# Optimization experiments

Hardware: AMD Instinct MI355X
Metric: run time of the kernel (lower is better)

The kernel has to match this reference:

```python
import jax, jax.numpy as jnp
import numpy as np

B, S, D = 16, 2048, 256

def setup_inputs() -> dict:
    key = jax.random.key(0)
    ks = jax.random.split(key, 7)
    scale = 1.0 / np.sqrt(D)
    return {
        "x": jax.random.normal(ks[0], (B, S, D), dtype=jnp.float32),
        "Wq": jax.random.normal(ks[1], (D, D), dtype=jnp.float32) * scale,
        "bq": jax.random.normal(ks[2], (D,), dtype=jnp.float32) * 0.01,
        "Wk": jax.random.normal(ks[3], (D, D), dtype=jnp.float32) * scale,
        "bk": jax.random.normal(ks[4], (D,), dtype=jnp.float32) * 0.01,
        "Wv": jax.random.normal(ks[5], (D, D), dtype=jnp.float32) * scale,
        "bv": jax.random.normal(ks[6], (D,), dtype=jnp.float32) * 0.01,
    }

def reference(x, Wq, bq, Wk, bk, Wv, bv):
    # q,k,v: [B,S,D]
    q = x @ Wq + bq
    k = x @ Wk + bk
    v = x @ Wv + bv
    inv_sqrt_d = jnp.asarray(1.0 / np.sqrt(x.shape[-1]), dtype=x.dtype)
    energy = jnp.einsum('bqd,bkd->bqk', q, k) * inv_sqrt_d  # [B,S,S]
    attn = jax.nn.softmax(energy, axis=-1)
    weighted = jnp.einsum('bqk,bkd->bqd', attn, v)  # [B,S,D]
    return weighted.sum(axis=1)  # [B,D]
```

## Files before the change

### kernel.cpp

```cpp
#include <hip/hip_runtime.h>
#include <hip/hip_bf16.h>

typedef __bf16 bf16_t;
typedef bf16_t bf16x8 __attribute__((ext_vector_type(8)));
typedef bf16_t bf16x4 __attribute__((ext_vector_type(4)));
typedef float  f32x4  __attribute__((ext_vector_type(4)));

constexpr int S = 2048, D = 256;


__device__ __forceinline__ float fast_exp2(float x) {
    return __builtin_amdgcn_exp2f(x);
}

__global__ void wt_kernel(const float* __restrict__ Wq, const float* __restrict__ Wk,
                          bf16_t* __restrict__ wtf) {
    int idx = blockIdx.x * 256 + threadIdx.x;
    int w    = idx >> 13;
    int rem  = idx & 8191;
    int nt   = rem >> 9;
    int rem2 = rem & 511;
    int ks   = rem2 >> 6;
    int lane = rem2 & 63;
    int lm = lane & 15, lg = lane >> 4;
    const float* Wsrc = (w == 0) ? Wq : Wk;
    int col = nt * 16 + lm, krow = ks * 32 + lg * 8;
    bf16x8 o;
#pragma unroll
    for (int j = 0; j < 8; j++) o[j] = (bf16_t)Wsrc[(krow + j) * 256 + col];
    *(bf16x8*)(wtf + (size_t)idx * 8) = o;
}

__global__ __launch_bounds__(256) void xconv_kernel(
    const float* __restrict__ x, bf16_t* __restrict__ xf) {
    __shared__ bf16_t xt[4][4096];
    int tid = threadIdx.x, wave = tid >> 6, lane = tid & 63;
    int qb = blockIdx.x * 4 + wave;
    const float* xr = x + (size_t)qb * 16 * 256;
    bf16_t* buf = xt[wave];
    int ks = lane >> 3, lg = (lane & 7) >> 1, j = (lane & 1) * 4;
#pragma unroll
    for (int rr = 0; rr < 16; rr++) {
        float4 f = *(const float4*)(xr + rr * 256 + lane * 4);
        bf16x4 o;
        o[0] = (bf16_t)f.x; o[1] = (bf16_t)f.y; o[2] = (bf16_t)f.z; o[3] = (bf16_t)f.w;
        *(bf16x4*)&buf[(ks * 64 + lg * 16 + rr) * 8 + j] = o;
    }
    bf16_t* dst = xf + (size_t)qb * 4096;
#pragma unroll
    for (int k2 = 0; k2 < 8; k2++) {
        bf16x8 v = *(const bf16x8*)&buf[k2 * 512 + lane * 8];
        *(bf16x8*)(dst + k2 * 512 + lane * 8) = v;
    }
}

__global__ __launch_bounds__(256, 2) void proj_kernel(
    const bf16_t* __restrict__ xf, const bf16_t* __restrict__ wtf,
    const float* __restrict__ bq, const float* __restrict__ bk,
    bf16_t* __restrict__ qo, bf16_t* __restrict__ ko) {
    __shared__ bf16_t bst[32768];
    __shared__ bf16_t sb_all[4][1152];
    int w    = blockIdx.y;
    int tid  = threadIdx.x;
    int wave = tid >> 6, lane = tid & 63, lm = lane & 15, lg = lane >> 4;
    int rowb = blockIdx.x >> 1;
    int colh = blockIdx.x & 1;
    int rowg = wave >> 1, colg = wave & 1;
    const float* bias = (w == 0) ? bq : bk;

    {
        const bf16_t* src = wtf + w * 65536 + (size_t)colh * 32768;
#pragma unroll
        for (int rnd = 0; rnd < 4; rnd++) {
            bf16x8 tmp[4];
#pragma unroll
            for (int u = 0; u < 4; u++)
                tmp[u] = *(const bf16x8*)(src + (size_t)((rnd * 4 + u) * 256 + tid) * 8);
#pragma unroll
            for (int u = 0; u < 4; u++)
                *(bf16x8*)&bst[(size_t)((rnd * 4 + u) * 256 + tid) * 8] = tmp[u];
        }
    }

    int qb0 = rowb * 8 + rowg * 4;
    bf16x8 af[4][8];
#pragma unroll
    for (int s = 0; s < 4; s++) {
        const bf16_t* ab = xf + (size_t)(qb0 + s) * 4096;
#pragma unroll
        for (int ks = 0; ks < 8; ks++)
            af[s][ks] = *(const bf16x8*)(ab + ks * 512 + lane * 8);
    }
    __syncthreads();

    f32x4 acc[4][4];
#pragma unroll
    for (int s = 0; s < 4; s++)
#pragma unroll
        for (int nt = 0; nt < 4; nt++) acc[s][nt] = f32x4{0.f, 0.f, 0.f, 0.f};
#pragma unroll
    for (int ks = 0; ks < 8; ks++) {
#pragma unroll
        for (int nt = 0; nt < 4; nt++) {
            bf16x8 bfr = *(const bf16x8*)&bst[(size_t)(((colg * 4 + nt) * 8 + ks) * 512) + lane * 8];
#pragma unroll
            for (int s = 0; s < 4; s++)
                acc[s][nt] = __builtin_amdgcn_mfma_f32_16x16x32_bf16(af[s][ks], bfr, acc[s][nt], 0, 0, 0);
        }
    }

    bf16_t* sb = sb_all[wave];
    bf16_t* dst = (w == 0) ? qo : ko;
    int c0 = colh * 128 + colg * 64;
#pragma unroll
    for (int s = 0; s < 4; s++) {
#pragma unroll
        for (int nt = 0; nt < 4; nt++) {
            int colloc = nt * 16 + lm;
            float bval = bias[c0 + colloc];
#pragma unroll
            for (int r = 0; r < 4; r++)
                sb[(lg * 4 + r) * 72 + colloc] = (bf16_t)(acc[s][nt][r] + bval);
        }
#pragma unroll
        for (int kk = 0; kk < 2; kk++) {
            bf16x8 v8 = *(const bf16x8*)&sb[lm * 72 + kk * 32 + lg * 8];
            *(bf16x8*)(dst + ((size_t)((qb0 + s) * 8 + (c0 >> 5) + kk)) * 512 + lane * 8) = v8;
        }
    }
}

template <int PASS>
__global__ __launch_bounds__(512, 2) void attn_pass(
    const bf16_t* __restrict__ q, const bf16_t* __restrict__ kmat,
    float* __restrict__ lpart, float* __restrict__ wpart) {
    __shared__ bf16_t wacc[8][512];

    int tid  = threadIdx.x;
    int wave = tid >> 6, lane = tid & 63, lm = lane & 15, lg = lane >> 4;
    int i    = blockIdx.x;
    int idx2 = i >> 3;
    int qt   = idx2 & 3;
    int kh   = (idx2 >> 2) & 3;
    int b    = (i & 7) * 2 + (idx2 >> 4);

    bf16x8 af[4][8];
#pragma unroll
    for (int s = 0; s < 4; s++) {
        const bf16_t* qb = q + ((size_t)((b * 128 + qt * 32 + wave * 4 + s) * 8)) * 512;
#pragma unroll
        for (int ks = 0; ks < 8; ks++)
            af[s][ks] = *(const bf16x8*)(qb + ks * 512 + lane * 8);
    }

    constexpr float SCL = 0.0625f * 1.44269504f;

    float lr[4][4];
    if (PASS == 2) {
#pragma unroll
        for (int s = 0; s < 4; s++)
#pragma unroll
            for (int r = 0; r < 4; r++) {
                int row = qt * 512 + wave * 64 + s * 16 + lg * 4 + r;
                float l = 0.f;
#pragma unroll
                for (int k2 = 0; k2 < 4; k2++)
                    l += lpart[(size_t)(k2 * 16 + b) * 2048 + row];
                lr[s][r] = -__builtin_log2f(l);
            }
    }

    float lsum[4][4];
#pragma unroll
    for (int s = 0; s < 4; s++)
#pragma unroll
        for (int r = 0; r < 4; r++) lsum[s][r] = 0.f;

    const bf16_t* kb_base = kmat + (size_t)(b * 128 + kh * 32) * 4096;

    for (int t = 0; t < 8; t++) {
#pragma unroll
        for (int h = 0; h < 2; h++) {
            f32x4 sacc[4][2];
#pragma unroll
            for (int s = 0; s < 4; s++) {
                sacc[s][0] = f32x4{0.f, 0.f, 0.f, 0.f};
                sacc[s][1] = f32x4{0.f, 0.f, 0.f, 0.f};
            }
#pragma unroll
            for (int ks = 0; ks < 8; ks++) {
                bf16x8 b0 = *(const bf16x8*)(kb_base + (size_t)((t * 4 + h * 2 + 0) * 8 + ks) * 512 + lane * 8);
                bf16x8 b1 = *(const bf16x8*)(kb_base + (size_t)((t * 4 + h * 2 + 1) * 8 + ks) * 512 + lane * 8);
#pragma unroll
                for (int s = 0; s < 4; s++) {
                    sacc[s][0] = __builtin_amdgcn_mfma_f32_16x16x32_bf16(af[s][ks], b0, sacc[s][0], 0, 0, 0);
                    sacc[s][1] = __builtin_amdgcn_mfma_f32_16x16x32_bf16(af[s][ks], b1, sacc[s][1], 0, 0, 0);
                }
            }
            if (PASS == 1) {
#pragma unroll
                for (int s = 0; s < 4; s++)
#pragma unroll
                    for (int j = 0; j < 2; j++)
#pragma unroll
                        for (int r = 0; r < 4; r++)
                            lsum[s][r] += fast_exp2(sacc[s][j][r] * SCL);
            } else {
#pragma unroll
                for (int j = 0; j < 2; j++) {
                    float wv = 0.f;
#pragma unroll
                    for (int s = 0; s < 4; s++)
#pragma unroll
                        for (int r = 0; r < 4; r++)
                            wv += fast_exp2(__builtin_fmaf(sacc[s][j][r], SCL, lr[s][r]));
                    wv += __shfl_xor(wv, 16);
                    wv += __shfl_xor(wv, 32);
                    if (lg == 0) wacc[wave][t * 64 + (h * 2 + j) * 16 + lm] = (bf16_t)wv;
                }
            }
        }
    }

    if (PASS == 1) {
#pragma unroll
        for (int s = 0; s < 4; s++)
#pragma unroll
            for (int r = 0; r < 4; r++) {
                float v2 = lsum[s][r];
                v2 += __shfl_xor(v2, 1);
                v2 += __shfl_xor(v2, 2);
                v2 += __shfl_xor(v2, 4);
                v2 += __shfl_xor(v2, 8);
                if (lm == 0) {
                    int row = qt * 512 + wave * 64 + s * 16 + lg * 4 + r;
                    lpart[(size_t)(kh * 16 + b) * 2048 + row] = v2;
                }
            }
    } else {
        __syncthreads();
        float sum = 0.f;
#pragma unroll
        for (int w2 = 0; w2 < 8; w2++) sum += (float)wacc[w2][tid];
        wpart[(size_t)(qt * 16 + b) * 2048 + kh * 512 + tid] = sum;
    }
}

__global__ __launch_bounds__(256) void xsum_kernel(
    const float* __restrict__ wpart, const float* __restrict__ x,
    float* __restrict__ gpart) {
    __shared__ float ldsw[128];
    int b = blockIdx.x >> 4, kseg = blockIdx.x & 15, tid = threadIdx.x;
    if (tid < 128) {
        int key = kseg * 128 + tid;
        float s = 0.f;
#pragma unroll
        for (int qt = 0; qt < 4; qt++) s += wpart[(size_t)(qt * 16 + b) * 2048 + key];
        ldsw[tid] = s;
    }
    __syncthreads();
    const float* xb = x + ((size_t)b * 2048 + kseg * 128) * 256;
    float acc = 0.f;
#pragma unroll 8
    for (int t = 0; t < 128; t++) acc += ldsw[t] * xb[(size_t)t * 256 + tid];
    gpart[(size_t)(kseg * 16 + b) * 256 + tid] = acc;
}

__global__ __launch_bounds__(256) void final_kernel(
    const float* __restrict__ gpart, const float* __restrict__ Wv,
    const float* __restrict__ bv, float* __restrict__ out) {
    __shared__ float yl[256];
    int b = blockIdx.x, tid = threadIdx.x;
    float s = 0.f;
#pragma unroll
    for (int ks = 0; ks < 16; ks++) s += gpart[(size_t)(ks * 16 + b) * 256 + tid];
    yl[tid] = s;
    __syncthreads();
    float acc = 0.f;
#pragma unroll 4
    for (int c = 0; c < 256; c++) acc += yl[c] * Wv[c * 256 + tid];
    out[b * 256 + tid] = acc + 2048.0f * bv[tid];
}

extern "C" void kernel_launch(void* const* d_in, const int* in_sizes, int n_in,
                              void* d_out, int out_size, void* d_ws, size_t ws_size,
                              hipStream_t stream) {
    const float* x  = (const float*)d_in[0];
    const float* Wq = (const float*)d_in[1];
    const float* bq = (const float*)d_in[2];
    const float* Wk = (const float*)d_in[3];
    const float* bk = (const float*)d_in[4];
    const float* Wv = (const float*)d_in[5];
    const float* bv = (const float*)d_in[6];
    float* out = (float*)d_out;

    char* ws = (char*)d_ws;
    bf16_t* wtf   = (bf16_t*)(ws);
    bf16_t* xf    = (bf16_t*)(ws + 262144);
    bf16_t* q     = (bf16_t*)(ws + 17039360);
    bf16_t* kmat  = (bf16_t*)(ws + 33816576);
    float*  lpart = (float*) (ws + 50593792);
    float*  wpart = (float*) (ws + 51118080);
    float*  gpart = (float*) (ws + 51642368);

    wt_kernel<<<dim3(64), dim3(256), 0, stream>>>(Wq, Wk, wtf);
    xconv_kernel<<<dim3(512), dim3(256), 0, stream>>>(x, xf);
    proj_kernel<<<dim3(512, 2), dim3(256), 0, stream>>>(xf, wtf, bq, bk, q, kmat);
    attn_pass<1><<<dim3(256), dim3(512), 0, stream>>>(q, kmat, lpart, wpart);
    attn_pass<2><<<dim3(256), dim3(512), 0, stream>>>(q, kmat, lpart, wpart);
    xsum_kernel<<<dim3(256), dim3(256), 0, stream>>>(wpart, x, gpart);
    final_kernel<<<dim3(16), dim3(256), 0, stream>>>(gpart, Wv, bv, out);
}
```

Before: 225.3 us.

## Fuse two attention passes into one kernel with per-block row sums

```diff
diff --git a/kernel.cpp b/kernel.cpp
--- a/kernel.cpp
+++ b/kernel.cpp
@@ -130,119 +130,122 @@
     }
 }
 
-template <int PASS>
-__global__ __launch_bounds__(512, 2) void attn_pass(
+__global__ __launch_bounds__(256) void attn_fused(
     const bf16_t* __restrict__ q, const bf16_t* __restrict__ kmat,
-    float* __restrict__ lpart, float* __restrict__ wpart) {
-    __shared__ bf16_t wacc[8][512];
+    float* __restrict__ wpart) {
+    __shared__ float lbuf[4][64];
 
     int tid  = threadIdx.x;
     int wave = tid >> 6, lane = tid & 63, lm = lane & 15, lg = lane >> 4;
     int i    = blockIdx.x;
-    int idx2 = i >> 3;
-    int qt   = idx2 & 3;
-    int kh   = (idx2 >> 2) & 3;
-    int b    = (i & 7) * 2 + (idx2 >> 4);
+    int b    = (i & 7) * 2 + ((i >> 8) & 1);
+    int qt   = (i >> 3) & 31;
 
     bf16x8 af[4][8];
 #pragma unroll
     for (int s = 0; s < 4; s++) {
-        const bf16_t* qb = q + ((size_t)((b * 128 + qt * 32 + wave * 4 + s) * 8)) * 512;
+        const bf16_t* qb = q + ((size_t)((b * 128 + qt * 4 + s) * 8)) * 512;
 #pragma unroll
         for (int ks = 0; ks < 8; ks++)
             af[s][ks] = *(const bf16x8*)(qb + ks * 512 + lane * 8);
     }
 
     constexpr float SCL = 0.0625f * 1.44269504f;
-
+    const bf16_t* kb = kmat + ((size_t)((b * 128 + wave * 32) * 8)) * 512;
+
+    float lsum[4][4];
+#pragma unroll
+    for (int s = 0; s < 4; s++)
+#pragma unroll
+        for (int r = 0; r < 4; r++) lsum[s][r] = 0.f;
+
+    {
+        bf16x8 cur[8], nxt[8];
+#pragma unroll
+        for (int u = 0; u < 8; u++)
+            cur[u] = *(const bf16x8*)(kb + u * 512 + lane * 8);
+        for (int t = 0; t < 32; t++) {
+            if (t < 31) {
+#pragma unroll
+                for (int u = 0; u < 8; u++)
+                    nxt[u] = *(const bf16x8*)(kb + (size_t)(t + 1) * 4096 + u * 512 + lane * 8);
+            }
+            f32x4 sacc[4];
+#pragma unroll
+            for (int s = 0; s < 4; s++) sacc[s] = f32x4{0.f, 0.f, 0.f, 0.f};
+#pragma unroll
+            for (int ks = 0; ks < 8; ks++)
+#pragma unroll
+                for (int s = 0; s < 4; s++)
+                    sacc[s] = __builtin_amdgcn_mfma_f32_16x16x32_bf16(af[s][ks], cur[ks], sacc[s], 0, 0, 0);
+#pragma unroll
+            for (int s = 0; s < 4; s++)
+#pragma unroll
+                for (int r = 0; r < 4; r++)
+                    lsum[s][r] += fast_exp2(sacc[s][r] * SCL);
+            if (t < 31) {
+#pragma unroll
+                for (int u = 0; u < 8; u++) cur[u] = nxt[u];
+            }
+        }
+    }
+
+#pragma unroll
+    for (int s = 0; s < 4; s++)
+#pragma unroll
+        for (int r = 0; r < 4; r++) {
+            float v2 = lsum[s][r];
+            v2 += __shfl_xor(v2, 1);
+            v2 += __shfl_xor(v2, 2);
+            v2 += __shfl_xor(v2, 4);
+            v2 += __shfl_xor(v2, 8);
+            if (lm == 0) lbuf[wave][s * 16 + lg * 4 + r] = v2;
+        }
+    __syncthreads();
     float lr[4][4];
-    if (PASS == 2) {
-#pragma unroll
-        for (int s = 0; s < 4; s++)
-#pragma unroll
-            for (int r = 0; r < 4; r++) {
-                int row = qt * 512 + wave * 64 + s * 16 + lg * 4 + r;
-                float l = 0.f;
-#pragma unroll
-                for (int k2 = 0; k2 < 4; k2++)
-                    l += lpart[(size_t)(k2 * 16 + b) * 2048 + row];
-                lr[s][r] = -__builtin_log2f(l);
+#pragma unroll
+    for (int s = 0; s < 4; s++)
+#pragma unroll
+        for (int r = 0; r < 4; r++) {
+            int row = s * 16 + lg * 4 + r;
+            float l = lbuf[0][row] + lbuf[1][row] + lbuf[2][row] + lbuf[3][row];
+            lr[s][r] = -__builtin_log2f(l);
+        }
+
+    {
+        float* wp = wpart + (size_t)(qt * 16 + b) * 2048 + wave * 512;
+        bf16x8 cur[8], nxt[8];
+#pragma unroll
+        for (int u = 0; u < 8; u++)
+            cur[u] = *(const bf16x8*)(kb + u * 512 + lane * 8);
+        for (int t = 0; t < 32; t++) {
+            if (t < 31) {
+#pragma unroll
+                for (int u = 0; u < 8; u++)
+                    nxt[u] = *(const bf16x8*)(kb + (size_t)(t + 1) * 4096 + u * 512 + lane * 8);
             }
-    }
-
-    float lsum[4][4];
-#pragma unroll
-    for (int s = 0; s < 4; s++)
-#pragma unroll
-        for (int r = 0; r < 4; r++) lsum[s][r] = 0.f;
-
-    const bf16_t* kb_base = kmat + (size_t)(b * 128 + kh * 32) * 4096;
-
-    for (int t = 0; t < 8; t++) {
-#pragma unroll
-        for (int h = 0; h < 2; h++) {
-            f32x4 sacc[4][2];
-#pragma unroll
-            for (int s = 0; s < 4; s++) {
-                sacc[s][0] = f32x4{0.f, 0.f, 0.f, 0.f};
-                sacc[s][1] = f32x4{0.f, 0.f, 0.f, 0.f};
+            f32x4 sacc[4];
+#pragma unroll
+            for (int s = 0; s < 4; s++) sacc[s] = f32x4{0.f, 0.f, 0.f, 0.f};
+#pragma unroll
+            for (int ks = 0; ks < 8; ks++)
+#pragma unroll
+                for (int s = 0; s < 4; s++)
+                    sacc[s] = __builtin_amdgcn_mfma_f32_16x16x32_bf16(af[s][ks], cur[ks], sacc[s], 0, 0, 0);
+            float wv = 0.f;
+#pragma unroll
+            for (int s = 0; s < 4; s++)
+#pragma unroll
+                for (int r = 0; r < 4; r++)
+                    wv += fast_exp2(__builtin_fmaf(sacc[s][r], SCL, lr[s][r]));
+            wv += __shfl_xor(wv, 16);
+            wv += __shfl_xor(wv, 32);
+            if (lg == 0) wp[t * 16 + lm] = wv;
+            if (t < 31) {
+#pragma unroll
+                for (int u = 0; u < 8; u++) cur[u] = nxt[u];
             }
-#pragma unroll
-            for (int ks = 0; ks < 8; ks++) {
-                bf16x8 b0 = *(const bf16x8*)(kb_base + (size_t)((t * 4 + h * 2 + 0) * 8 + ks) * 512 + lane * 8);
-                bf16x8 b1 = *(const bf16x8*)(kb_base + (size_t)((t * 4 + h * 2 + 1) * 8 + ks) * 512 + lane * 8);
-#pragma unroll
-                for (int s = 0; s < 4; s++) {
-                    sacc[s][0] = __builtin_amdgcn_mfma_f32_16x16x32_bf16(af[s][ks], b0, sacc[s][0], 0, 0, 0);
-                    sacc[s][1] = __builtin_amdgcn_mfma_f32_16x16x32_bf16(af[s][ks], b1, sacc[s][1], 0, 0, 0);
-                }
-            }
-            if (PASS == 1) {
-#pragma unroll
-                for (int s = 0; s < 4; s++)
-#pragma unroll
-                    for (int j = 0; j < 2; j++)
-#pragma unroll
-                        for (int r = 0; r < 4; r++)
-                            lsum[s][r] += fast_exp2(sacc[s][j][r] * SCL);
-            } else {
-#pragma unroll
-                for (int j = 0; j < 2; j++) {
-                    float wv = 0.f;
-#pragma unroll
-                    for (int s = 0; s < 4; s++)
-#pragma unroll
-                        for (int r = 0; r < 4; r++)
-                            wv += fast_exp2(__builtin_fmaf(sacc[s][j][r], SCL, lr[s][r]));
-                    wv += __shfl_xor(wv, 16);
-                    wv += __shfl_xor(wv, 32);
-                    if (lg == 0) wacc[wave][t * 64 + (h * 2 + j) * 16 + lm] = (bf16_t)wv;
-                }
-            }
-        }
-    }
-
-    if (PASS == 1) {
-#pragma unroll
-        for (int s = 0; s < 4; s++)
-#pragma unroll
-            for (int r = 0; r < 4; r++) {
-                float v2 = lsum[s][r];
-                v2 += __shfl_xor(v2, 1);
-                v2 += __shfl_xor(v2, 2);
-                v2 += __shfl_xor(v2, 4);
-                v2 += __shfl_xor(v2, 8);
-                if (lm == 0) {
-                    int row = qt * 512 + wave * 64 + s * 16 + lg * 4 + r;
-                    lpart[(size_t)(kh * 16 + b) * 2048 + row] = v2;
-                }
-            }
-    } else {
-        __syncthreads();
-        float sum = 0.f;
-#pragma unroll
-        for (int w2 = 0; w2 < 8; w2++) sum += (float)wacc[w2][tid];
-        wpart[(size_t)(qt * 16 + b) * 2048 + kh * 512 + tid] = sum;
+        }
     }
 }
 
@@ -254,8 +257,7 @@
     if (tid < 128) {
         int key = kseg * 128 + tid;
         float s = 0.f;
-#pragma unroll
-        for (int qt = 0; qt < 4; qt++) s += wpart[(size_t)(qt * 16 + b) * 2048 + key];
+        for (int qt = 0; qt < 32; qt++) s += wpart[(size_t)(qt * 16 + b) * 2048 + key];
         ldsw[tid] = s;
     }
     __syncthreads();
@@ -299,15 +301,13 @@
     bf16_t* xf    = (bf16_t*)(ws + 262144);
     bf16_t* q     = (bf16_t*)(ws + 17039360);
     bf16_t* kmat  = (bf16_t*)(ws + 33816576);
-    float*  lpart = (float*) (ws + 50593792);
-    float*  wpart = (float*) (ws + 51118080);
-    float*  gpart = (float*) (ws + 51642368);
+    float*  wpart = (float*) (ws + 50593792);
+    float*  gpart = (float*) (ws + 54788096);
 
     wt_kernel<<<dim3(64), dim3(256), 0, stream>>>(Wq, Wk, wtf);
     xconv_kernel<<<dim3(512), dim3(256), 0, stream>>>(x, xf);
     proj_kernel<<<dim3(512, 2), dim3(256), 0, stream>>>(xf, wtf, bq, bk, q, kmat);
-    attn_pass<1><<<dim3(256), dim3(512), 0, stream>>>(q, kmat, lpart, wpart);
-    attn_pass<2><<<dim3(256), dim3(512), 0, stream>>>(q, kmat, lpart, wpart);
+    attn_fused<<<dim3(512), dim3(256), 0, stream>>>(q, kmat, wpart);
     xsum_kernel<<<dim3(256), dim3(256), 0, stream>>>(wpart, x, gpart);
     final_kernel<<<dim3(16), dim3(256), 0, stream>>>(gpart, Wv, bv, out);
 }
```

New measurement: 194.2 us. -13.8%, faster.
